# Optimization experiments

Measured on AMD Instinct MI355X. Metric: run time of the kernel, lower is better.

## Reference

```python
import jax, jax.numpy as jnp
import numpy as np
from jax import lax

N_QUBITS = 10
N_LAYERS = 6
DIM = 1 << N_QUBITS
EPS = 1e-5

_i = np.arange(DIM)
# Z_SIGNS[w, i] = (+1/-1) eigenvalue of PauliZ on wire w (wire 0 = most significant bit)
Z_SIGNS = jnp.asarray(np.stack([1.0 - 2.0 * ((_i >> (N_QUBITS - 1 - w)) & 1) for w in range(N_QUBITS)]).astype(np.float32))

def _layer_perm(r):
    # composed permutation of the ring of CNOT(w, (w+r)%n) gates of one StronglyEntanglingLayers layer
    p = _i.copy()
    for w in range(N_QUBITS):
        c, t = w, (w + r) % N_QUBITS
        pc, pt = N_QUBITS - 1 - c, N_QUBITS - 1 - t
        pg = _i ^ (((_i >> pc) & 1) << pt)
        p = p[pg]
    return p

LAYER_PERMS = [jnp.asarray(_layer_perm(l % (N_QUBITS - 1) + 1), dtype=jnp.int32) for l in range(N_LAYERS)]

def _apply_1q(state, U, wire):
    # state: (B, DIM) complex64; U: (2,2) or batched (B,2,2)
    B = state.shape[0]
    left = 1 << wire
    right = DIM // (2 * left)
    s = state.reshape(B, left, 2, right)
    if U.ndim == 3:
        out = jnp.einsum('bij,bljr->blir', U, s)
    else:
        out = jnp.einsum('ij,bljr->blir', U, s)
    return out.reshape(B, DIM)

def _ry_batched(theta):
    c = jnp.cos(theta / 2)
    s = jnp.sin(theta / 2)
    return jnp.stack([jnp.stack([c, -s], -1), jnp.stack([s, c], -1)], -2).astype(jnp.complex64)

def _rot(phi, theta, omega):
    # PennyLane Rot(phi, theta, omega) = RZ(omega) @ RY(theta) @ RZ(phi)
    c = jnp.cos(theta / 2)
    s = jnp.sin(theta / 2)
    m00 = jnp.exp(-1j * (phi + omega) / 2) * c
    m01 = -jnp.exp(1j * (phi - omega) / 2) * s
    m10 = jnp.exp(-1j * (phi - omega) / 2) * s
    m11 = jnp.exp(1j * (phi + omega) / 2) * c
    return jnp.stack([jnp.stack([m00, m01]), jnp.stack([m10, m11])]).astype(jnp.complex64)

def quantum_forward(xq, qw):
    # batched statevector simulation of: RY(pi*x_i) encoding + StronglyEntanglingLayers
    B = xq.shape[0]
    state = jnp.zeros((B, DIM), jnp.complex64).at[:, 0].set(1.0)
    for w in range(N_QUBITS):
        state = _apply_1q(state, _ry_batched(jnp.pi * xq[:, w]), w)
    for l in range(N_LAYERS):
        for w in range(N_QUBITS):
            state = _apply_1q(state, _rot(qw[l, w, 0], qw[l, w, 1], qw[l, w, 2]), w)
        state = state[:, LAYER_PERMS[l]]
    probs = state.real ** 2 + state.imag ** 2
    return probs @ Z_SIGNS.T  # (B, N_QUBITS) expvals of PauliZ

def _conv(x, w, b):
    y = lax.conv_general_dilated(x, w, (1, 1), 'SAME', dimension_numbers=('NCHW', 'OIHW', 'NCHW'))
    return y + b[None, :, None, None]

def _bn(x, g, b):
    # BatchNorm2d in training mode: per-batch statistics over (N, H, W)
    m = jnp.mean(x, (0, 2, 3), keepdims=True)
    v = jnp.var(x, (0, 2, 3), keepdims=True)
    return (x - m) * lax.rsqrt(v + EPS) * g[None, :, None, None] + b[None, :, None, None]

def _pool(x):
    return lax.reduce_window(x, -jnp.inf, lax.max, (1, 1, 2, 2), (1, 1, 2, 2), 'VALID')

def setup_inputs() -> dict:
    key = jax.random.key(0)
    ks = jax.random.split(key, 16)
    n = lambda k, sh, sc: jax.random.normal(k, sh, jnp.float32) * sc
    return {
        'x': jax.random.normal(ks[0], (256, 3, 64, 64), jnp.float32),
        'conv1_w': n(ks[1], (32, 3, 3, 3), 0.1), 'conv1_b': jnp.zeros(32),
        'bn1_g': jnp.ones(32), 'bn1_b': jnp.zeros(32),
        'conv2_w': n(ks[2], (32, 32, 3, 3), 0.05), 'conv2_b': jnp.zeros(32),
        'bn2_g': jnp.ones(32), 'bn2_b': jnp.zeros(32),
        'conv3_w': n(ks[3], (64, 32, 3, 3), 0.05), 'conv3_b': jnp.zeros(64),
        'bn3_g': jnp.ones(64), 'bn3_b': jnp.zeros(64),
        'conv4_w': n(ks[4], (64, 64, 3, 3), 0.05), 'conv4_b': jnp.zeros(64),
        'bn4_g': jnp.ones(64), 'bn4_b': jnp.zeros(64),
        'fc1_w': n(ks[5], (128, 64 * 16 * 16), 0.01), 'fc1_b': jnp.zeros(128),
        'fc2_w': n(ks[6], (10, 128), 0.05), 'fc2_b': jnp.zeros(10),
        'q_weights': jax.random.uniform(ks[7], (6, 10, 3), jnp.float32),
        'head_w': n(ks[8], (10, 10), 0.1), 'head_b': jnp.zeros(10),
    }

def reference(x, conv1_w, conv1_b, bn1_g, bn1_b, conv2_w, conv2_b, bn2_g, bn2_b,
              conv3_w, conv3_b, bn3_g, bn3_b, conv4_w, conv4_b, bn4_g, bn4_b,
              fc1_w, fc1_b, fc2_w, fc2_b, q_weights, head_w, head_b):
    h = jax.nn.relu(_bn(_conv(x, conv1_w, conv1_b), bn1_g, bn1_b))
    h = jax.nn.relu(_bn(_conv(h, conv2_w, conv2_b), bn2_g, bn2_b))
    h = _pool(h)  # Dropout(0.25) is identity in eval
    h = jax.nn.relu(_bn(_conv(h, conv3_w, conv3_b), bn3_g, bn3_b))
    h = jax.nn.relu(_bn(_conv(h, conv4_w, conv4_b), bn4_g, bn4_b))
    h = _pool(h)
    h = h.reshape(h.shape[0], -1)  # (B, 64*16*16)
    h = jax.nn.relu(h @ fc1_w.T + fc1_b)
    h = h @ fc2_w.T + fc2_b  # (B, n_qubits)
    q = quantum_forward(h, q_weights)
    return q @ head_w.T + head_b  # (B, num_classes)
```

## Files before the change

kernel.cpp:

```cpp
#include <hip/hip_runtime.h>
#include <math.h>

#define PI_F 3.14159265358979323846f

typedef __attribute__((ext_vector_type(8))) _Float16 half8;
typedef __attribute__((ext_vector_type(4))) _Float16 half4;
typedef __attribute__((ext_vector_type(4))) float f32x4;

__global__ __launch_bounds__(256) void x_to_nhwc4_kernel(
    const float* __restrict__ x, _Float16* __restrict__ X4)
{
    int idx = blockIdx.x * 256 + threadIdx.x;
    int n = idx >> 11;
    int p = (idx & 2047) * 2;
    const float* xb = x + (size_t)n * 12288;
    float2 c0 = *(const float2*)&xb[p];
    float2 c1 = *(const float2*)&xb[4096 + p];
    float2 c2 = *(const float2*)&xb[8192 + p];
    half8 o;
    o[0] = (_Float16)c0.x; o[1] = (_Float16)c1.x; o[2] = (_Float16)c2.x; o[3] = (_Float16)0.f;
    o[4] = (_Float16)c0.y; o[5] = (_Float16)c1.y; o[6] = (_Float16)c2.y; o[7] = (_Float16)0.f;
    *(half8*)&X4[(size_t)idx * 8] = o;
}

__global__ __launch_bounds__(256) void wt_transform_kernel(
    const float* __restrict__ w1, const float* __restrict__ w2,
    const float* __restrict__ w3, const float* __restrict__ w4,
    _Float16* __restrict__ t1, _Float16* __restrict__ t2,
    _Float16* __restrict__ t3, _Float16* __restrict__ t4)
{
    int idx = blockIdx.x * 256 + threadIdx.x;
    if (idx < 9216) {
        int j = idx & 7, co = (idx >> 3) & 31, k8 = idx >> 8;
        int k = k8 * 8 + j, tap = k >> 5, ci = k & 31;
        t2[idx] = (_Float16)w2[(size_t)(co * 32 + ci) * 9 + tap];
    } else if (idx < 27648) {
        int e = idx - 9216;
        int j = e & 7, co = (e >> 3) & 31, r = e >> 8;
        int k8 = r % 36, gg = r / 36;
        int k = k8 * 8 + j, tap = k >> 5, ci = k & 31;
        t3[e] = (_Float16)w3[(size_t)((gg * 32 + co) * 32 + ci) * 9 + tap];
    } else if (idx < 64512) {
        int e = idx - 27648;
        int j = e & 7, co = (e >> 3) & 31, r = e >> 8;
        int k8 = r % 36, gc = r / 36;
        int g = gc >> 1, cc = gc & 1;
        int kl = k8 * 8 + j, tap = kl >> 5, ci = cc * 32 + (kl & 31);
        t4[e] = (_Float16)w4[(size_t)((g * 32 + co) * 64 + ci) * 9 + tap];
    } else if (idx < 66560) {
        int e = idx - 64512;
        int j = e & 7, co = (e >> 3) & 31, k8 = e >> 8;
        int k = k8 * 8 + j, tap = k >> 2, ci = k & 3;
        t1[e] = (_Float16)((tap < 9 && ci < 3) ? w1[(size_t)(co * 3 + ci) * 9 + tap] : 0.f);
    }
}

__global__ __launch_bounds__(256) void fc1w_transform_kernel(
    const float* __restrict__ w, _Float16* __restrict__ wt)
{
    __shared__ float lds[64][65];
    const int t = threadIdx.x;
    const int yx0 = blockIdx.x * 64;
    const int j = blockIdx.y;
    #pragma unroll
    for (int i = 0; i < 16; ++i) {
        int idx = t + 256 * i;
        int c = idx >> 6, yxl = idx & 63;
        lds[c][yxl] = w[(size_t)j * 16384 + c * 256 + yx0 + yxl];
    }
    __syncthreads();
    #pragma unroll
    for (int i = 0; i < 2; ++i) {
        int idx = t + 256 * i;
        int yxl = idx >> 3, c8 = idx & 7;
        half8 h;
        #pragma unroll
        for (int jj = 0; jj < 8; ++jj)
            h[jj] = (_Float16)lds[c8 * 8 + jj][yxl];
        *(half8*)&wt[(size_t)j * 16384 + (size_t)(yx0 + yxl) * 64 + c8 * 8] = h;
    }
}

__global__ __launch_bounds__(256) void quantum_prep_kernel(
    const float* __restrict__ qw, float* __restrict__ rotm,
    unsigned short* __restrict__ perm)
{
    int t = threadIdx.x;
    if (t < 60) {
        float phi = qw[t * 3], th = qw[t * 3 + 1], om = qw[t * 3 + 2];
        float c = cosf(0.5f * th), s = sinf(0.5f * th);
        float apo = 0.5f * (phi + om), amo = 0.5f * (phi - om);
        float cpo = cosf(apo), spo = sinf(apo);
        float cmo = cosf(amo), smo = sinf(amo);
        rotm[t * 8 + 0] = cpo * c;  rotm[t * 8 + 1] = -spo * c;
        rotm[t * 8 + 2] = -cmo * s; rotm[t * 8 + 3] = -smo * s;
        rotm[t * 8 + 4] = cmo * s;  rotm[t * 8 + 5] = -smo * s;
        rotm[t * 8 + 6] = cpo * c;  rotm[t * 8 + 7] = spo * c;
    }
    for (int e = t; e < 6144; e += 256) {
        int layer = e >> 10, i = e & 1023;
        int r = layer % 9 + 1;
        int jdx = i;
        for (int w = 9; w >= 0; --w) {
            int tt = (w + r) % 10;
            int pc = 9 - w, pt_ = 9 - tt;
            jdx ^= ((jdx >> pc) & 1) << pt_;
        }
        perm[e] = (unsigned short)jdx;
    }
}

__global__ __launch_bounds__(256) void conv1_stats_kernel(
    const _Float16* __restrict__ X4, const _Float16* __restrict__ w1m,
    const float* __restrict__ bias, float* __restrict__ partials)
{
    constexpr int TC = 66, TR = 6;
    constexpr int NPIX = (TR + 1) * TC;
    __shared__ __align__(16) _Float16 s_in[NPIX * 4];
    __shared__ __align__(16) _Float16 s_w[2048];
    __shared__ float s_red[64];

    const int t = threadIdx.x;
    const int row0 = blockIdx.x * 4;
    const int n = blockIdx.z;

    *(half8*)&s_w[t * 8] = *(const half8*)&w1m[t * 8];

    for (int p = t; p < NPIX; p += 256) {
        int col = p % TC, r = p / TC;
        int gy = row0 + r - 1, gx = col - 1;
        uint2 u = make_uint2(0u, 0u);
        if (r < TR && gy >= 0 && gy < 64 && gx >= 0 && gx < 64)
            u = *(const uint2*)&X4[(((size_t)n << 12) + (gy << 6) + gx) * 4];
        *(uint2*)&s_in[p * 4] = u;
    }
    if (t < 64) s_red[t] = 0.f;
    __syncthreads();

    const int w = t >> 6, l = t & 63;
    const int lm = l & 15, lg = l >> 4;
    int pA[4];
    #pragma unroll
    for (int f = 0; f < 4; ++f) {
        int m = w * 64 + f * 16 + lm;
        pA[f] = (m >> 6) * TC + (m & 63);
    }
    f32x4 zero4 = {0.f, 0.f, 0.f, 0.f};
    f32x4 acc[4][2];
    #pragma unroll
    for (int f = 0; f < 4; ++f) { acc[f][0] = zero4; acc[f][1] = zero4; }

    {
        const int t0 = lg * 2;
        const int off0 = (t0 / 3) * TC + (t0 % 3);
        const int off1 = ((t0 + 1) / 3) * TC + ((t0 + 1) % 3);
        half8 b0 = *(const half8*)&s_w[(lg * 32 + lm) * 8];
        half8 b1 = *(const half8*)&s_w[(lg * 32 + 16 + lm) * 8];
        #pragma unroll
        for (int f = 0; f < 4; ++f) {
            half4 alo = *(const half4*)&s_in[(pA[f] + off0) * 4];
            half4 ahi = *(const half4*)&s_in[(pA[f] + off1) * 4];
            half8 a;
            #pragma unroll
            for (int j = 0; j < 4; ++j) { a[j] = alo[j]; a[4 + j] = ahi[j]; }
            acc[f][0] = __builtin_amdgcn_mfma_f32_16x16x32_f16(a, b0, acc[f][0], 0, 0, 0);
            acc[f][1] = __builtin_amdgcn_mfma_f32_16x16x32_f16(a, b1, acc[f][1], 0, 0, 0);
        }
    }
    {
        half8 b0 = *(const half8*)&s_w[((4 + lg) * 32 + lm) * 8];
        half8 b1 = *(const half8*)&s_w[((4 + lg) * 32 + 16 + lm) * 8];
        #pragma unroll
        for (int f = 0; f < 4; ++f) {
            half8 a;
            #pragma unroll
            for (int j = 0; j < 8; ++j) a[j] = (_Float16)0.f;
            if (lg == 0) {
                half4 alo = *(const half4*)&s_in[(pA[f] + 134) * 4];
                half4 ahi = *(const half4*)&s_in[(pA[f] + 198) * 4];
                #pragma unroll
                for (int j = 0; j < 4; ++j) { a[j] = alo[j]; a[4 + j] = ahi[j]; }
            }
            acc[f][0] = __builtin_amdgcn_mfma_f32_16x16x32_f16(a, b0, acc[f][0], 0, 0, 0);
            acc[f][1] = __builtin_amdgcn_mfma_f32_16x16x32_f16(a, b1, acc[f][1], 0, 0, 0);
        }
    }

    float bv0 = bias[lm];
    float bv1 = bias[16 + lm];
    float s0 = 0.f, s20 = 0.f, s1 = 0.f, s21 = 0.f;
    #pragma unroll
    for (int f = 0; f < 4; ++f) {
        #pragma unroll
        for (int r = 0; r < 4; ++r) {
            float v0 = acc[f][0][r] + bv0;
            float v1 = acc[f][1][r] + bv1;
            s0 += v0; s20 += v0 * v0;
            s1 += v1; s21 += v1 * v1;
        }
    }
    s0 += __shfl_xor(s0, 16);  s0 += __shfl_xor(s0, 32);
    s1 += __shfl_xor(s1, 16);  s1 += __shfl_xor(s1, 32);
    s20 += __shfl_xor(s20, 16); s20 += __shfl_xor(s20, 32);
    s21 += __shfl_xor(s21, 16); s21 += __shfl_xor(s21, 32);
    if (l < 16) {
        atomicAdd(&s_red[lm], s0);
        atomicAdd(&s_red[16 + lm], s1);
        atomicAdd(&s_red[32 + lm], s20);
        atomicAdd(&s_red[48 + lm], s21);
    }
    __syncthreads();
    if (t < 64)
        partials[((size_t)n * 16 + blockIdx.x) * 64 + t] = s_red[t];
}

__global__ __launch_bounds__(256, 2) void conv2_fused_kernel(
    const _Float16* __restrict__ X4, const _Float16* __restrict__ w1m,
    const float* __restrict__ c1bias, const _Float16* __restrict__ ssh1,
    const _Float16* __restrict__ wt2, const float* __restrict__ c2bias,
    _Float16* __restrict__ out0, _Float16* __restrict__ out1,
    float* __restrict__ partials)
{
    constexpr int W = 64, COUT = 32, MF = 8, NB = 2;
    constexpr int SPW = MF * 16;
    constexpr int ROWS = 8;
    constexpr int TR = 10, TC = 66, NPIX = TR * TC;
    constexpr int KC = 288;
    constexpr int XC = 68, XROWS = 14, XPIX = XROWS * XC;
    __shared__ __align__(16) _Float16 s_in[NPIX * 32];
    __shared__ __align__(16) _Float16 s_x4[XPIX * 4];
    __shared__ __align__(16) _Float16 s_w1[2048];
    __shared__ float s_red[64];

    const int t = threadIdx.x;
    const int row0 = blockIdx.x * ROWS;
    const int n = blockIdx.z;
    const int w = t >> 6, l = t & 63;
    const int lm = l & 15, lg = l >> 4;

    *(half8*)&s_w1[t * 8] = *(const half8*)&w1m[t * 8];
    for (int p = t; p < XPIX; p += 256) {
        int c = p % XC, r = p / XC;
        int gy = row0 - 2 + r, gx = c - 2;
        uint2 u = make_uint2(0u, 0u);
        if (r < 12 && gy >= 0 && gy < 64 && gx >= 0 && gx < 64)
            u = *(const uint2*)&X4[(((size_t)n << 12) + (gy << 6) + gx) * 4];
        *(uint2*)&s_x4[p * 4] = u;
    }
    if (t < 64) s_red[t] = 0.f;
    __syncthreads();

    {
        const float b1v0 = c1bias[lm], b1v1 = c1bias[16 + lm];
        const _Float16 sc0 = ssh1[lm], sh0 = ssh1[32 + lm];
        const _Float16 sc1 = ssh1[16 + lm], sh1 = ssh1[48 + lm];
        const int c8a = lm >> 3, ja = lm & 7;
        for (int g = w; g < 42; g += 4) {
            int py = g * 16 + lm;
            int ry = py / 66, cy = py - ry * 66;
            int pb = ry * XC + cy;
            f32x4 a0 = {0.f, 0.f, 0.f, 0.f}, a1 = {0.f, 0.f, 0.f, 0.f};
            {
                const int t0 = lg * 2;
                const int off0 = (t0 / 3) * XC + (t0 % 3);
                const int off1 = ((t0 + 1) / 3) * XC + ((t0 + 1) % 3);
                half8 b0 = *(const half8*)&s_w1[(lg * 32 + lm) * 8];
                half8 b1 = *(const half8*)&s_w1[(lg * 32 + 16 + lm) * 8];
                half4 alo = *(const half4*)&s_x4[(pb + off0) * 4];
                half4 ahi = *(const half4*)&s_x4[(pb + off1) * 4];
                half8 a;
                #pragma unroll
                for (int j = 0; j < 4; ++j) { a[j] = alo[j]; a[4 + j] = ahi[j]; }
                a0 = __builtin_amdgcn_mfma_f32_16x16x32_f16(a, b0, a0, 0, 0, 0);
                a1 = __builtin_amdgcn_mfma_f32_16x16x32_f16(a, b1, a1, 0, 0, 0);
            }
            {
                half8 b0 = *(const half8*)&s_w1[((4 + lg) * 32 + lm) * 8];
                half8 b1 = *(const half8*)&s_w1[((4 + lg) * 32 + 16 + lm) * 8];
                half8 a;
                #pragma unroll
                for (int j = 0; j < 8; ++j) a[j] = (_Float16)0.f;
                if (lg == 0) {
                    half4 alo = *(const half4*)&s_x4[(pb + 138) * 4];
                    half4 ahi = *(const half4*)&s_x4[(pb + 204) * 4];
                    #pragma unroll
                    for (int j = 0; j < 4; ++j) { a[j] = alo[j]; a[4 + j] = ahi[j]; }
                }
                a0 = __builtin_amdgcn_mfma_f32_16x16x32_f16(a, b0, a0, 0, 0, 0);
                a1 = __builtin_amdgcn_mfma_f32_16x16x32_f16(a, b1, a1, 0, 0, 0);
            }
            #pragma unroll
            for (int r2 = 0; r2 < 4; ++r2) {
                int py2 = g * 16 + lg * 4 + r2;
                if (py2 < NPIX) {
                    int r2y = py2 / 66, c2y = py2 - r2y * 66;
                    int gy = row0 - 1 + r2y, gx = c2y - 1;
                    _Float16 y0 = (_Float16)0.f, y1 = (_Float16)0.f;
                    if (gy >= 0 && gy < 64 && gx >= 0 && gx < 64) {
                        _Float16 v0 = (_Float16)(a0[r2] + b1v0);
                        _Float16 v1 = (_Float16)(a1[r2] + b1v1);
                        _Float16 f0 = v0 * sc0 + sh0;
                        _Float16 f1 = v1 * sc1 + sh1;
                        y0 = f0 > (_Float16)0.f ? f0 : (_Float16)0.f;
                        y1 = f1 > (_Float16)0.f ? f1 : (_Float16)0.f;
                    }
                    s_in[(c8a * NPIX + py2) * 8 + ja] = y0;
                    s_in[((2 + c8a) * NPIX + py2) * 8 + ja] = y1;
                }
            }
        }
    }
    __syncthreads();

    int pA[MF];
    #pragma unroll
    for (int f = 0; f < MF; ++f) {
        int m = w * SPW + f * 16 + lm;
        pA[f] = (m / W) * TC + (m % W);
    }
    f32x4 zero4 = {0.f, 0.f, 0.f, 0.f};
    f32x4 acc[MF][NB];
    #pragma unroll
    for (int f = 0; f < MF; ++f)
        #pragma unroll
        for (int nb = 0; nb < NB; ++nb) acc[f][nb] = zero4;

    #pragma unroll
    for (int tap = 0; tap < 9; ++tap) {
        const int dy = tap / 3, dx = tap % 3;
        const int poff = dy * TC + dx;
        half8 b[NB];
        #pragma unroll
        for (int nb = 0; nb < NB; ++nb) {
            int col = nb * 16 + lm;
            b[nb] = *(const half8*)&wt2[((tap * 4 + lg) * 32 + col) * 8];
        }
        #pragma unroll
        for (int f = 0; f < MF; ++f) {
            half8 a = *(const half8*)&s_in[(lg * NPIX + pA[f] + poff) * 8];
            #pragma unroll
            for (int nb = 0; nb < NB; ++nb)
                acc[f][nb] = __builtin_amdgcn_mfma_f32_16x16x32_f16(a, b[nb], acc[f][nb], 0, 0, 0);
        }
    }

    float bv[NB], s[NB], s2[NB];
    #pragma unroll
    for (int nb = 0; nb < NB; ++nb) {
        bv[nb] = c2bias[nb * 16 + lm];
        s[nb] = 0.f; s2[nb] = 0.f;
    }
    #pragma unroll
    for (int f = 0; f < MF; ++f) {
        #pragma unroll
        for (int r = 0; r < 4; ++r) {
            #pragma unroll
            for (int nb = 0; nb < NB; ++nb) {
                float v = acc[f][nb][r] + bv[nb];
                s[nb] += v; s2[nb] += v * v;
            }
        }
    }
    #pragma unroll
    for (int nb = 0; nb < NB; ++nb) {
        s[nb] += __shfl_xor(s[nb], 16);  s[nb] += __shfl_xor(s[nb], 32);
        s2[nb] += __shfl_xor(s2[nb], 16); s2[nb] += __shfl_xor(s2[nb], 32);
    }
    if (l < 16) {
        #pragma unroll
        for (int nb = 0; nb < NB; ++nb) {
            atomicAdd(&s_red[nb * 16 + lm], s[nb]);
            atomicAdd(&s_red[32 + nb * 16 + lm], s2[nb]);
        }
    }

    {
        constexpr int FH = MF / 2;
        constexpr int PPIX = (ROWS / 2) * (W / 2);
        __syncthreads();
        _Float16* pk = s_in;
        #pragma unroll
        for (int nb = 0; nb < NB; ++nb) {
            #pragma unroll
            for (int f = 0; f < FH; ++f) {
                #pragma unroll
                for (int rp = 0; rp < 2; ++rp) {
                    float a0 = acc[f][nb][2 * rp] + bv[nb];
                    float a1 = acc[f][nb][2 * rp + 1] + bv[nb];
                    float a2 = acc[f + FH][nb][2 * rp] + bv[nb];
                    float a3 = acc[f + FH][nb][2 * rp + 1] + bv[nb];
                    float mn = fminf(fminf(a0, a1), fminf(a2, a3));
                    float mx = fmaxf(fmaxf(a0, a1), fmaxf(a2, a3));
                    int xp = f * 8 + lg * 2 + rp;
                    int o = (w * (W / 2) + xp) * COUT + nb * 16 + lm;
                    pk[o] = (_Float16)mn;
                    pk[PPIX * COUT + o] = (_Float16)mx;
                }
            }
        }
        __syncthreads();
        size_t gb = (((size_t)n * 32 + (row0 >> 1)) * 32) * COUT;
        for (int idx = t; idx < PPIX * COUT / 8; idx += 256) {
            *(half8*)&out0[gb + (size_t)idx * 8] = *(const half8*)&pk[idx * 8];
            *(half8*)&out1[gb + (size_t)idx * 8] = *(const half8*)&pk[PPIX * COUT + idx * 8];
        }
    }

    __syncthreads();
    if (t < 64) {
        size_t bid = (size_t)n * gridDim.x + blockIdx.x;
        partials[bid * 64 + t] = s_red[t];
    }
}

template<int BLOCK, int W, int CIN, int COUT, int MF, int NB,
         bool MMIN, bool POOL>
__global__ __launch_bounds__(BLOCK, (BLOCK == 512 ? 4 : 3)) void conv_mfma_kernel(
    const _Float16* __restrict__ in0, const _Float16* __restrict__ in1,
    const _Float16* __restrict__ coef, const _Float16* __restrict__ wt,
    const float* __restrict__ bias,
    _Float16* __restrict__ out0, _Float16* __restrict__ out1,
    float* __restrict__ partials)
{
    constexpr int H = W;
    constexpr int NWAVE = BLOCK / 64;
    constexpr int SPW = MF * 16;
    constexpr int ROWS = NWAVE * SPW / W;
    constexpr int TR = ROWS + 2;
    constexpr int TC = W + 2;
    constexpr int NPIX = TR * TC;
    constexpr int NCH = CIN / 32;
    constexpr int C8N = CIN / 8;
    constexpr int KC = 288;
    constexpr int COUTB = NB * 16;
    __shared__ __align__(16) _Float16 s_in[NPIX * CIN];
    __shared__ float s_red[2 * COUTB];

    const int t = threadIdx.x;
    const int row0 = blockIdx.x * ROWS;
    const int n = blockIdx.z;

    const int w = t >> 6, l = t & 63;
    const int lm = l & 15, lg = l >> 4;
    int pA[MF];
    #pragma unroll
    for (int f = 0; f < MF; ++f) {
        int m = w * SPW + f * 16 + lm;
        pA[f] = (m / W) * TC + (m % W);
    }
    f32x4 zero4 = {0.f, 0.f, 0.f, 0.f};
    f32x4 acc[MF][NB];
    #pragma unroll
    for (int f = 0; f < MF; ++f)
        #pragma unroll
        for (int nb = 0; nb < NB; ++nb) acc[f][nb] = zero4;
    if (t < 2 * COUTB) s_red[t] = 0.f;

    for (int idx = t; idx < NPIX * C8N; idx += BLOCK) {
        int c8 = idx % C8N;
        int p = idx / C8N;
        int col = p % TC, r = p / TC;
        int gy = row0 + r - 1, gx = col - 1;
        half8 v;
        #pragma unroll
        for (int j = 0; j < 8; ++j) v[j] = (_Float16)0.f;
        if (gy >= 0 && gy < H && gx >= 0 && gx < W) {
            size_t gidx = (((size_t)n * H + gy) * W + gx) * CIN + c8 * 8;
            if (MMIN) {
                half8 mn = *(const half8*)&in0[gidx];
                half8 mx = *(const half8*)&in1[gidx];
                half8 sa = *(const half8*)&coef[c8 * 8];
                half8 sb = *(const half8*)&coef[CIN + c8 * 8];
                half8 sh = *(const half8*)&coef[2 * CIN + c8 * 8];
                #pragma unroll
                for (int j = 0; j < 8; ++j) {
                    _Float16 f = mx[j] * sa[j] + mn[j] * sb[j] + sh[j];
                    v[j] = f > (_Float16)0.f ? f : (_Float16)0.f;
                }
            } else {
                v = *(const half8*)&in0[gidx];
                if (coef) {
                    half8 sc = *(const half8*)&coef[c8 * 8];
                    half8 sh = *(const half8*)&coef[CIN + c8 * 8];
                    #pragma unroll
                    for (int j = 0; j < 8; ++j) {
                        _Float16 f = v[j] * sc[j] + sh[j];
                        v[j] = f > (_Float16)0.f ? f : (_Float16)0.f;
                    }
                }
            }
        }
        *(half8*)&s_in[(c8 * NPIX + p) * 8] = v;
    }
    __syncthreads();

    #pragma unroll
    for (int tap = 0; tap < 9; ++tap) {
        const int dy = tap / 3, dx = tap % 3;
        const int poff = dy * TC + dx;
        #pragma unroll
        for (int cc = 0; cc < NCH; ++cc) {
            half8 b[NB];
            #pragma unroll
            for (int nb = 0; nb < NB; ++nb) {
                int cog = nb * 16 + lm;
                int gg = cog >> 5, col = cog & 31;
                const _Float16* wp = wt + (size_t)(gg * NCH + cc) * KC * 32;
                b[nb] = *(const half8*)&wp[((tap * 4 + lg) * 32 + col) * 8];
            }
            #pragma unroll
            for (int f = 0; f < MF; ++f) {
                half8 a = *(const half8*)&s_in[((cc * 4 + lg) * NPIX + pA[f] + poff) * 8];
                #pragma unroll
                for (int nb = 0; nb < NB; ++nb)
                    acc[f][nb] = __builtin_amdgcn_mfma_f32_16x16x32_f16(a, b[nb], acc[f][nb], 0, 0, 0);
            }
        }
    }

    float bv[NB], s[NB], s2[NB];
    #pragma unroll
    for (int nb = 0; nb < NB; ++nb) {
        bv[nb] = bias[nb * 16 + lm];
        s[nb] = 0.f; s2[nb] = 0.f;
    }
    #pragma unroll
    for (int f = 0; f < MF; ++f) {
        #pragma unroll
        for (int r = 0; r < 4; ++r) {
            int m = w * SPW + f * 16 + lg * 4 + r;
            int yy = row0 + m / W, xo = m % W;
            size_t base = (((size_t)n * H + yy) * W + xo) * COUT;
            #pragma unroll
            for (int nb = 0; nb < NB; ++nb) {
                float v = acc[f][nb][r] + bv[nb];
                if (!POOL) out0[base + nb * 16 + lm] = (_Float16)v;
                s[nb] += v; s2[nb] += v * v;
            }
        }
    }
    #pragma unroll
    for (int nb = 0; nb < NB; ++nb) {
        s[nb] += __shfl_xor(s[nb], 16);  s[nb] += __shfl_xor(s[nb], 32);
        s2[nb] += __shfl_xor(s2[nb], 16); s2[nb] += __shfl_xor(s2[nb], 32);
    }
    if (l < 16) {
        #pragma unroll
        for (int nb = 0; nb < NB; ++nb) {
            atomicAdd(&s_red[nb * 16 + lm], s[nb]);
            atomicAdd(&s_red[COUTB + nb * 16 + lm], s2[nb]);
        }
    }

    if (POOL) {
        constexpr int FH = MF / 2;
        constexpr int PPIX = (ROWS / 2) * (W / 2);
        static_assert(2 * PPIX * COUT <= NPIX * CIN, "pool pack fits in s_in");
        __syncthreads();
        _Float16* pk = s_in;
        #pragma unroll
        for (int nb = 0; nb < NB; ++nb) {
            #pragma unroll
            for (int f = 0; f < FH; ++f) {
                #pragma unroll
                for (int rp = 0; rp < 2; ++rp) {
                    float a0 = acc[f][nb][2 * rp] + bv[nb];
                    float a1 = acc[f][nb][2 * rp + 1] + bv[nb];
                    float a2 = acc[f + FH][nb][2 * rp] + bv[nb];
                    float a3 = acc[f + FH][nb][2 * rp + 1] + bv[nb];
                    float mn = fminf(fminf(a0, a1), fminf(a2, a3));
                    float mx = fmaxf(fmaxf(a0, a1), fmaxf(a2, a3));
                    int xp = f * 8 + lg * 2 + rp;
                    int o = (w * (W / 2) + xp) * COUT + nb * 16 + lm;
                    pk[o] = (_Float16)mn;
                    pk[PPIX * COUT + o] = (_Float16)mx;
                }
            }
        }
        __syncthreads();
        size_t gb = (((size_t)n * (H / 2) + (row0 >> 1)) * (W / 2)) * COUT;
        for (int idx = t; idx < PPIX * COUT / 8; idx += BLOCK) {
            *(half8*)&out0[gb + (size_t)idx * 8] = *(const half8*)&pk[idx * 8];
            *(half8*)&out1[gb + (size_t)idx * 8] = *(const half8*)&pk[(PPIX * COUT + idx * 8)];
        }
    }

    __syncthreads();
    if (t < 2 * COUTB) {
        size_t bid = (size_t)n * gridDim.x + blockIdx.x;
        partials[bid * 2 * COUTB + t] = s_red[t];
    }
}

__global__ __launch_bounds__(256) void bn_finalize_kernel(
    const float* __restrict__ partials, int nx, float inv_count,
    const float* __restrict__ gamma, const float* __restrict__ beta,
    float* __restrict__ ss, _Float16* __restrict__ ssh,
    _Float16* __restrict__ sab, int COUT)
{
    const int c = blockIdx.x;
    const int t = threadIdx.x;
    float sum = 0.f, sq = 0.f;
    int total = 256 * nx;
    for (int e = t; e < total; e += 256) {
        size_t off = (size_t)e * 2 * COUT;
        sum += partials[off + c];
        sq  += partials[off + COUT + c];
    }
    #pragma unroll
    for (int off = 32; off > 0; off >>= 1) {
        sum += __shfl_xor(sum, off);
        sq  += __shfl_xor(sq, off);
    }
    __shared__ float rs[4], rq[4];
    if ((t & 63) == 0) { rs[t >> 6] = sum; rq[t >> 6] = sq; }
    __syncthreads();
    if (t == 0) {
        sum = rs[0] + rs[1] + rs[2] + rs[3];
        sq  = rq[0] + rq[1] + rq[2] + rq[3];
        float mean = sum * inv_count;
        float var = sq * inv_count - mean * mean;
        float scale = gamma[c] * rsqrtf(var + 1e-5f);
        float shift = beta[c] - mean * scale;
        ss[c] = scale;
        ss[COUT + c] = shift;
        if (ssh) {
            ssh[c] = (_Float16)scale;
            ssh[COUT + c] = (_Float16)shift;
        }
        if (sab) {
            sab[c] = (_Float16)(scale > 0.f ? scale : 0.f);
            sab[COUT + c] = (_Float16)(scale > 0.f ? 0.f : scale);
            sab[2 * COUT + c] = (_Float16)shift;
        }
    }
}

__global__ __launch_bounds__(256) void fc1_mfma_kernel(
    const _Float16* __restrict__ Amin, const _Float16* __restrict__ Amax,
    const _Float16* __restrict__ sab, const _Float16* __restrict__ Bw,
    float* __restrict__ hp)
{
    __shared__ __align__(16) _Float16 As[64][72];
    __shared__ __align__(16) _Float16 Bs[128][72];
    const int t = threadIdx.x;
    const int mt = blockIdx.x;
    const int kc = blockIdx.y;
    const int w = t >> 6, l = t & 63;
    const int lm = l & 15, lg = l >> 4;

    f32x4 zero4 = {0.f, 0.f, 0.f, 0.f};
    f32x4 acc[8];
    #pragma unroll
    for (int nb = 0; nb < 8; ++nb) acc[nb] = zero4;

    const size_t a_base = (size_t)(mt * 64) * 16384 + (size_t)kc * 512;
    const size_t b_base = (size_t)kc * 512;

    for (int p = 0; p < 8; ++p) {
        __syncthreads();
        #pragma unroll
        for (int i = 0; i < 2; ++i) {
            int idx = t + 256 * i;
            int r = idx >> 3, c8 = idx & 7;
            size_t off = a_base + (size_t)r * 16384 + p * 64 + c8 * 8;
            half8 mn = *(const half8*)&Amin[off];
            half8 mx = *(const half8*)&Amax[off];
            half8 sa = *(const half8*)&sab[c8 * 8];
            half8 sb = *(const half8*)&sab[64 + c8 * 8];
            half8 sh = *(const half8*)&sab[128 + c8 * 8];
            half8 v;
            #pragma unroll
            for (int j = 0; j < 8; ++j) {
                _Float16 f = mx[j] * sa[j] + mn[j] * sb[j] + sh[j];
                v[j] = f > (_Float16)0.f ? f : (_Float16)0.f;
            }
            *(half8*)&As[r][c8 * 8] = v;
        }
        #pragma unroll
        for (int i = 0; i < 4; ++i) {
            int idx = t + 256 * i;
            int r = idx >> 3, c8 = idx & 7;
            *(half8*)&Bs[r][c8 * 8] =
                *(const half8*)&Bw[b_base + (size_t)r * 16384 + p * 64 + c8 * 8];
        }
        __syncthreads();
        #pragma unroll
        for (int ks = 0; ks < 64; ks += 32) {
            half8 a = *(const half8*)&As[w * 16 + lm][ks + lg * 8];
            #pragma unroll
            for (int nb = 0; nb < 8; ++nb) {
                half8 b = *(const half8*)&Bs[nb * 16 + lm][ks + lg * 8];
                acc[nb] = __builtin_amdgcn_mfma_f32_16x16x32_f16(a, b, acc[nb], 0, 0, 0);
            }
        }
    }
    #pragma unroll
    for (int nb = 0; nb < 8; ++nb) {
        #pragma unroll
        for (int r = 0; r < 4; ++r) {
            int row = mt * 64 + w * 16 + lg * 4 + r;
            hp[((size_t)kc * 256 + row) * 128 + nb * 16 + lm] = acc[nb][r];
        }
    }
}

__global__ __launch_bounds__(256) void fc1_reduce_kernel(
    const float* __restrict__ hp, const float* __restrict__ bias, float* __restrict__ h1)
{
    int gid = blockIdx.x * 256 + threadIdx.x;
    int n = gid >> 7, j = gid & 127;
    float s = bias[j];
    #pragma unroll
    for (int kc = 0; kc < 32; ++kc) s += hp[((size_t)kc * 256 + n) * 128 + j];
    h1[gid] = fmaxf(0.f, s);
}

__global__ __launch_bounds__(64) void fc2_kernel(
    const float* __restrict__ h1, const float* __restrict__ w,
    const float* __restrict__ b, float* __restrict__ xq)
{
    int n = blockIdx.x, l = threadIdx.x;
    float a0 = h1[n * 128 + l], a1 = h1[n * 128 + 64 + l];
    float p[10];
    #pragma unroll
    for (int j = 0; j < 10; ++j)
        p[j] = w[j * 128 + l] * a0 + w[j * 128 + 64 + l] * a1;
    #pragma unroll
    for (int j = 0; j < 10; ++j) {
        #pragma unroll
        for (int off = 32; off > 0; off >>= 1) p[j] += __shfl_xor(p[j], off);
    }
    if (l == 0) {
        #pragma unroll
        for (int j = 0; j < 10; ++j) xq[n * 10 + j] = p[j] + b[j];
    }
}

__global__ __launch_bounds__(64) void quantum_head_kernel(
    const float* __restrict__ xq, const float* __restrict__ rotm,
    const unsigned short* __restrict__ perm,
    const float* __restrict__ head_w, const float* __restrict__ head_b,
    float* __restrict__ outp)
{
    __shared__ float lds[2048];
    const int n = blockIdx.x;
    const int l = threadIdx.x;

    float ar[16], ai[16];
    #pragma unroll
    for (int r = 0; r < 16; ++r) { ar[r] = 0.f; ai[r] = 0.f; }
    if (l == 0) ar[0] = 1.f;

    #pragma unroll
    for (int w = 0; w < 10; ++w) {
        float th = 0.5f * PI_F * xq[n * 10 + w];
        float c = cosf(th), s = sinf(th);
        const int k = 9 - w;
        if (k >= 6) {
            const int b = k - 6;
            #pragma unroll
            for (int r = 0; r < 16; ++r) {
                if (!(r & (1 << b))) {
                    int r1 = r | (1 << b);
                    float a0 = ar[r], a1 = ar[r1];
                    ar[r]  = c * a0 - s * a1;
                    ar[r1] = s * a0 + c * a1;
                }
            }
        } else {
            float ss = ((l >> k) & 1) ? s : -s;
            #pragma unroll
            for (int r = 0; r < 16; ++r) {
                float p = __shfl_xor(ar[r], 1 << k);
                ar[r] = c * ar[r] + ss * p;
            }
        }
    }

    #pragma unroll 1
    for (int layer = 0; layer < 6; ++layer) {
        #pragma unroll
        for (int w = 0; w < 10; ++w) {
            const float* m = rotm + (layer * 10 + w) * 8;
            float m00r = m[0], m00i = m[1], m01r = m[2], m01i = m[3];
            float m10r = m[4], m10i = m[5], m11r = m[6], m11i = m[7];
            const int k = 9 - w;
            if (k >= 6) {
                const int b = k - 6;
                #pragma unroll
                for (int r = 0; r < 16; ++r) {
                    if (!(r & (1 << b))) {
                        int r1 = r | (1 << b);
                        float a0r = ar[r], a0i = ai[r];
                        float a1r = ar[r1], a1i = ai[r1];
                        ar[r]  = m00r * a0r - m00i * a0i + m01r * a1r - m01i * a1i;
                        ai[r]  = m00r * a0i + m00i * a0r + m01r * a1i + m01i * a1r;
                        ar[r1] = m10r * a0r - m10i * a0i + m11r * a1r - m11i * a1i;
                        ai[r1] = m10r * a0i + m10i * a0r + m11r * a1i + m11i * a1r;
                    }
                }
            } else {
                int bit = (l >> k) & 1;
                float mAr = bit ? m11r : m00r, mAi = bit ? m11i : m00i;
                float mBr = bit ? m10r : m01r, mBi = bit ? m10i : m01i;
                #pragma unroll
                for (int r = 0; r < 16; ++r) {
                    float pr = __shfl_xor(ar[r], 1 << k);
                    float pi = __shfl_xor(ai[r], 1 << k);
                    float mr = ar[r], mi = ai[r];
                    ar[r] = mAr * mr - mAi * mi + mBr * pr - mBi * pi;
                    ai[r] = mAr * mi + mAi * mr + mBr * pi + mBi * pr;
                }
            }
        }
        #pragma unroll
        for (int r = 0; r < 16; ++r) {
            lds[(r << 6) | l] = ar[r];
            lds[1024 + ((r << 6) | l)] = ai[r];
        }
        __syncthreads();
        const unsigned short* pt = perm + layer * 1024;
        #pragma unroll
        for (int r = 0; r < 16; ++r) {
            int ji = pt[(r << 6) | l];
            ar[r] = lds[ji];
            ai[r] = lds[1024 + ji];
        }
        __syncthreads();
    }

    float S = 0.f, T0 = 0.f, T1 = 0.f, T2 = 0.f, T3 = 0.f;
    #pragma unroll
    for (int r = 0; r < 16; ++r) {
        float pr = ar[r] * ar[r] + ai[r] * ai[r];
        S += pr;
        T0 += (r & 1) ? -pr : pr;
        T1 += (r & 2) ? -pr : pr;
        T2 += (r & 4) ? -pr : pr;
        T3 += (r & 8) ? -pr : pr;
    }
    float pk[10];
    pk[0] = T3; pk[1] = T2; pk[2] = T1; pk[3] = T0;
    #pragma unroll
    for (int w = 4; w < 10; ++w)
        pk[w] = ((l >> (9 - w)) & 1) ? -S : S;
    #pragma unroll
    for (int w = 0; w < 10; ++w) {
        #pragma unroll
        for (int off = 1; off < 64; off <<= 1)
            pk[w] += __shfl_xor(pk[w], off);
    }
    if (l < 10) {
        float o = head_b[l];
        #pragma unroll
        for (int kk = 0; kk < 10; ++kk) o += pk[kk] * head_w[l * 10 + kk];
        outp[n * 10 + l] = o;
    }
}

extern "C" void kernel_launch(void* const* d_in, const int* in_sizes, int n_in,
                              void* d_out, int out_size, void* d_ws, size_t ws_size,
                              hipStream_t stream)
{
    const float* x   = (const float*)d_in[0];
    const float* c1w = (const float*)d_in[1];  const float* c1b = (const float*)d_in[2];
    const float* g1  = (const float*)d_in[3];  const float* b1  = (const float*)d_in[4];
    const float* c2w = (const float*)d_in[5];  const float* c2b = (const float*)d_in[6];
    const float* g2  = (const float*)d_in[7];  const float* b2  = (const float*)d_in[8];
    const float* c3w = (const float*)d_in[9];  const float* c3b = (const float*)d_in[10];
    const float* g3  = (const float*)d_in[11]; const float* b3  = (const float*)d_in[12];
    const float* c4w = (const float*)d_in[13]; const float* c4b = (const float*)d_in[14];
    const float* g4  = (const float*)d_in[15]; const float* b4  = (const float*)d_in[16];
    const float* f1w = (const float*)d_in[17]; const float* f1b = (const float*)d_in[18];
    const float* f2w = (const float*)d_in[19]; const float* f2b = (const float*)d_in[20];
    const float* qw  = (const float*)d_in[21];
    const float* hw  = (const float*)d_in[22]; const float* hb  = (const float*)d_in[23];

    float* ws = (float*)d_ws;
    _Float16* H0 = (_Float16*)ws;
    _Float16* H1 = H0 + 33554432;
    float* part = ws + 33554432;
    float* ss1  = part + 524288;
    float* ss2  = ss1 + 64;
    float* ss3  = ss2 + 64;
    float* ss4  = ss3 + 128;
    float* hp   = ss4 + 128;
    float* h1   = hp + 1048576;
    float* xqv  = h1 + 32768;
    float* rotm = xqv + 2560;
    unsigned short* perm16 = (unsigned short*)(rotm + 480);
    _Float16* ssh1 = (_Float16*)(perm16 + 6144);
    _Float16* ssh3 = ssh1 + 64;
    _Float16* sab2 = ssh3 + 128;
    _Float16* sab4 = sab2 + 96;
    _Float16* wt2  = sab4 + 192;
    _Float16* wt3  = wt2 + 9216;
    _Float16* wt4  = wt3 + 18432;
    _Float16* w1m  = wt4 + 36864;
    _Float16* w1t  = w1m + 2048;
    _Float16* X4   = w1t + 2097152;

    _Float16* minT2 = H1;
    _Float16* maxT2 = H1 + 8388608;
    _Float16* minT4 = H1;
    _Float16* maxT4 = H1 + 4194304;

    quantum_prep_kernel<<<1, 256, 0, stream>>>(qw, rotm, perm16);
    wt_transform_kernel<<<260, 256, 0, stream>>>(c1w, c2w, c3w, c4w, w1m, wt2, wt3, wt4);
    fc1w_transform_kernel<<<dim3(4, 128), 256, 0, stream>>>(f1w, w1t);
    x_to_nhwc4_kernel<<<2048, 256, 0, stream>>>(x, X4);

    conv1_stats_kernel<<<dim3(16, 1, 256), 256, 0, stream>>>(X4, w1m, c1b, part);
    bn_finalize_kernel<<<32, 256, 0, stream>>>(part, 16, 1.f / 1048576.f,
                                               g1, b1, ss1, ssh1, nullptr, 32);

    conv2_fused_kernel<<<dim3(8, 1, 256), 256, 0, stream>>>(
        X4, w1m, c1b, ssh1, wt2, c2b, minT2, maxT2, part);
    bn_finalize_kernel<<<32, 256, 0, stream>>>(part, 8, 1.f / 1048576.f,
                                               g2, b2, ss2, nullptr, sab2, 32);

    conv_mfma_kernel<512, 32, 32, 64, 4, 4, true, false>
        <<<dim3(2, 1, 256), 512, 0, stream>>>(
        minT2, maxT2, sab2, wt3, c3b, H0, nullptr, part);
    bn_finalize_kernel<<<64, 256, 0, stream>>>(part, 2, 1.f / 262144.f,
                                               g3, b3, ss3, ssh3, nullptr, 64);

    conv_mfma_kernel<512, 32, 64, 64, 4, 4, false, true>
        <<<dim3(2, 1, 256), 512, 0, stream>>>(
        H0, nullptr, ssh3, wt4, c4b, minT4, maxT4, part);
    bn_finalize_kernel<<<64, 256, 0, stream>>>(part, 2, 1.f / 262144.f,
                                               g4, b4, ss4, nullptr, sab4, 64);

    fc1_mfma_kernel<<<dim3(4, 32), 256, 0, stream>>>(minT4, maxT4, sab4, w1t, hp);
    fc1_reduce_kernel<<<128, 256, 0, stream>>>(hp, f1b, h1);

    fc2_kernel<<<256, 64, 0, stream>>>(h1, f2w, f2b, xqv);

    quantum_head_kernel<<<256, 64, 0, stream>>>(xqv, rotm, perm16, hw, hb, (float*)d_out);
}
```

Baseline: 214.6 us.

## Merge prep kernels, fuse fc1-reduce with fc2, and halve conv2 row tiles

Four preprocessing kernels become one launch that branches on block index, and the fc1 reduction and fc2 are fused into one kernel with LDS staging, removing three launches and the h1 round trip. The fused conv2 kernel now handles 4 rows per block instead of 8, with a smaller LDS footprint and launch bounds raised to 4 blocks per CU, doubling the grid. The 2x2 pooling is split into a horizontal min/max in registers and a vertical min/max during the store. Smaller tiles add halo recompute of conv1 and increase partial-statistic rows in exchange for higher occupancy.

```diff
diff --git a/kernel.cpp b/kernel.cpp
--- a/kernel.cpp
+++ b/kernel.cpp
@@ -7,106 +7,100 @@
 typedef __attribute__((ext_vector_type(4))) _Float16 half4;
 typedef __attribute__((ext_vector_type(4))) float f32x4;
 
-__global__ __launch_bounds__(256) void x_to_nhwc4_kernel(
-    const float* __restrict__ x, _Float16* __restrict__ X4)
-{
-    int idx = blockIdx.x * 256 + threadIdx.x;
-    int n = idx >> 11;
-    int p = (idx & 2047) * 2;
-    const float* xb = x + (size_t)n * 12288;
-    float2 c0 = *(const float2*)&xb[p];
-    float2 c1 = *(const float2*)&xb[4096 + p];
-    float2 c2 = *(const float2*)&xb[8192 + p];
-    half8 o;
-    o[0] = (_Float16)c0.x; o[1] = (_Float16)c1.x; o[2] = (_Float16)c2.x; o[3] = (_Float16)0.f;
-    o[4] = (_Float16)c0.y; o[5] = (_Float16)c1.y; o[6] = (_Float16)c2.y; o[7] = (_Float16)0.f;
-    *(half8*)&X4[(size_t)idx * 8] = o;
-}
-
-__global__ __launch_bounds__(256) void wt_transform_kernel(
+__global__ __launch_bounds__(256) void prep_kernel(
+    const float* __restrict__ x, _Float16* __restrict__ X4,
     const float* __restrict__ w1, const float* __restrict__ w2,
     const float* __restrict__ w3, const float* __restrict__ w4,
     _Float16* __restrict__ t1, _Float16* __restrict__ t2,
-    _Float16* __restrict__ t3, _Float16* __restrict__ t4)
-{
-    int idx = blockIdx.x * 256 + threadIdx.x;
-    if (idx < 9216) {
-        int j = idx & 7, co = (idx >> 3) & 31, k8 = idx >> 8;
-        int k = k8 * 8 + j, tap = k >> 5, ci = k & 31;
-        t2[idx] = (_Float16)w2[(size_t)(co * 32 + ci) * 9 + tap];
-    } else if (idx < 27648) {
-        int e = idx - 9216;
-        int j = e & 7, co = (e >> 3) & 31, r = e >> 8;
-        int k8 = r % 36, gg = r / 36;
-        int k = k8 * 8 + j, tap = k >> 5, ci = k & 31;
-        t3[e] = (_Float16)w3[(size_t)((gg * 32 + co) * 32 + ci) * 9 + tap];
-    } else if (idx < 64512) {
-        int e = idx - 27648;
-        int j = e & 7, co = (e >> 3) & 31, r = e >> 8;
-        int k8 = r % 36, gc = r / 36;
-        int g = gc >> 1, cc = gc & 1;
-        int kl = k8 * 8 + j, tap = kl >> 5, ci = cc * 32 + (kl & 31);
-        t4[e] = (_Float16)w4[(size_t)((g * 32 + co) * 64 + ci) * 9 + tap];
-    } else if (idx < 66560) {
-        int e = idx - 64512;
-        int j = e & 7, co = (e >> 3) & 31, k8 = e >> 8;
-        int k = k8 * 8 + j, tap = k >> 2, ci = k & 3;
-        t1[e] = (_Float16)((tap < 9 && ci < 3) ? w1[(size_t)(co * 3 + ci) * 9 + tap] : 0.f);
-    }
-}
-
-__global__ __launch_bounds__(256) void fc1w_transform_kernel(
-    const float* __restrict__ w, _Float16* __restrict__ wt)
-{
-    __shared__ float lds[64][65];
-    const int t = threadIdx.x;
-    const int yx0 = blockIdx.x * 64;
-    const int j = blockIdx.y;
-    #pragma unroll
-    for (int i = 0; i < 16; ++i) {
-        int idx = t + 256 * i;
-        int c = idx >> 6, yxl = idx & 63;
-        lds[c][yxl] = w[(size_t)j * 16384 + c * 256 + yx0 + yxl];
-    }
-    __syncthreads();
-    #pragma unroll
-    for (int i = 0; i < 2; ++i) {
-        int idx = t + 256 * i;
-        int yxl = idx >> 3, c8 = idx & 7;
-        half8 h;
-        #pragma unroll
-        for (int jj = 0; jj < 8; ++jj)
-            h[jj] = (_Float16)lds[c8 * 8 + jj][yxl];
-        *(half8*)&wt[(size_t)j * 16384 + (size_t)(yx0 + yxl) * 64 + c8 * 8] = h;
-    }
-}
-
-__global__ __launch_bounds__(256) void quantum_prep_kernel(
+    _Float16* __restrict__ t3, _Float16* __restrict__ t4,
+    const float* __restrict__ f1w, _Float16* __restrict__ w1t,
     const float* __restrict__ qw, float* __restrict__ rotm,
     unsigned short* __restrict__ perm)
 {
-    int t = threadIdx.x;
-    if (t < 60) {
-        float phi = qw[t * 3], th = qw[t * 3 + 1], om = qw[t * 3 + 2];
-        float c = cosf(0.5f * th), s = sinf(0.5f * th);
-        float apo = 0.5f * (phi + om), amo = 0.5f * (phi - om);
-        float cpo = cosf(apo), spo = sinf(apo);
-        float cmo = cosf(amo), smo = sinf(amo);
-        rotm[t * 8 + 0] = cpo * c;  rotm[t * 8 + 1] = -spo * c;
-        rotm[t * 8 + 2] = -cmo * s; rotm[t * 8 + 3] = -smo * s;
-        rotm[t * 8 + 4] = cmo * s;  rotm[t * 8 + 5] = -smo * s;
-        rotm[t * 8 + 6] = cpo * c;  rotm[t * 8 + 7] = spo * c;
-    }
-    for (int e = t; e < 6144; e += 256) {
-        int layer = e >> 10, i = e & 1023;
-        int r = layer % 9 + 1;
-        int jdx = i;
-        for (int w = 9; w >= 0; --w) {
-            int tt = (w + r) % 10;
-            int pc = 9 - w, pt_ = 9 - tt;
-            jdx ^= ((jdx >> pc) & 1) << pt_;
-        }
-        perm[e] = (unsigned short)jdx;
+    const int b = blockIdx.x;
+    const int t = threadIdx.x;
+    if (b < 2048) {
+        int idx = b * 256 + t;
+        int n = idx >> 11;
+        int p = (idx & 2047) * 2;
+        const float* xb = x + (size_t)n * 12288;
+        float2 c0 = *(const float2*)&xb[p];
+        float2 c1 = *(const float2*)&xb[4096 + p];
+        float2 c2 = *(const float2*)&xb[8192 + p];
+        half8 o;
+        o[0] = (_Float16)c0.x; o[1] = (_Float16)c1.x; o[2] = (_Float16)c2.x; o[3] = (_Float16)0.f;
+        o[4] = (_Float16)c0.y; o[5] = (_Float16)c1.y; o[6] = (_Float16)c2.y; o[7] = (_Float16)0.f;
+        *(half8*)&X4[(size_t)idx * 8] = o;
+    } else if (b < 2308) {
+        int idx = (b - 2048) * 256 + t;
+        if (idx < 9216) {
+            int j = idx & 7, co = (idx >> 3) & 31, k8 = idx >> 8;
+            int k = k8 * 8 + j, tap = k >> 5, ci = k & 31;
+            t2[idx] = (_Float16)w2[(size_t)(co * 32 + ci) * 9 + tap];
+        } else if (idx < 27648) {
+            int e = idx - 9216;
+            int j = e & 7, co = (e >> 3) & 31, r = e >> 8;
+            int k8 = r % 36, gg = r / 36;
+            int k = k8 * 8 + j, tap = k >> 5, ci = k & 31;
+            t3[e] = (_Float16)w3[(size_t)((gg * 32 + co) * 32 + ci) * 9 + tap];
+        } else if (idx < 64512) {
+            int e = idx - 27648;
+            int j = e & 7, co = (e >> 3) & 31, r = e >> 8;
+            int k8 = r % 36, gc = r / 36;
+            int g = gc >> 1, cc = gc & 1;
+            int kl = k8 * 8 + j, tap = kl >> 5, ci = cc * 32 + (kl & 31);
+            t4[e] = (_Float16)w4[(size_t)((g * 32 + co) * 64 + ci) * 9 + tap];
+        } else if (idx < 66560) {
+            int e = idx - 64512;
+            int j = e & 7, co = (e >> 3) & 31, k8 = e >> 8;
+            int k = k8 * 8 + j, tap = k >> 2, ci = k & 3;
+            t1[e] = (_Float16)((tap < 9 && ci < 3) ? w1[(size_t)(co * 3 + ci) * 9 + tap] : 0.f);
+        }
+    } else if (b < 2820) {
+        __shared__ float lds[64][65];
+        int b2 = b - 2308;
+        const int yx0 = (b2 & 3) * 64;
+        const int j = b2 >> 2;
+        #pragma unroll
+        for (int i = 0; i < 16; ++i) {
+            int idx = t + 256 * i;
+            int c = idx >> 6, yxl = idx & 63;
+            lds[c][yxl] = f1w[(size_t)j * 16384 + c * 256 + yx0 + yxl];
+        }
+        __syncthreads();
+        #pragma unroll
+        for (int i = 0; i < 2; ++i) {
+            int idx = t + 256 * i;
+            int yxl = idx >> 3, c8 = idx & 7;
+            half8 h;
+            #pragma unroll
+            for (int jj = 0; jj < 8; ++jj)
+                h[jj] = (_Float16)lds[c8 * 8 + jj][yxl];
+            *(half8*)&w1t[(size_t)j * 16384 + (size_t)(yx0 + yxl) * 64 + c8 * 8] = h;
+        }
+    } else {
+        if (t < 60) {
+            float phi = qw[t * 3], th = qw[t * 3 + 1], om = qw[t * 3 + 2];
+            float c = cosf(0.5f * th), s = sinf(0.5f * th);
+            float apo = 0.5f * (phi + om), amo = 0.5f * (phi - om);
+            float cpo = cosf(apo), spo = sinf(apo);
+            float cmo = cosf(amo), smo = sinf(amo);
+            rotm[t * 8 + 0] = cpo * c;  rotm[t * 8 + 1] = -spo * c;
+            rotm[t * 8 + 2] = -cmo * s; rotm[t * 8 + 3] = -smo * s;
+            rotm[t * 8 + 4] = cmo * s;  rotm[t * 8 + 5] = -smo * s;
+            rotm[t * 8 + 6] = cpo * c;  rotm[t * 8 + 7] = spo * c;
+        }
+        for (int e = t; e < 6144; e += 256) {
+            int layer = e >> 10, i = e & 1023;
+            int r = layer % 9 + 1;
+            int jdx = i;
+            for (int w = 9; w >= 0; --w) {
+                int tt = (w + r) % 10;
+                int pc = 9 - w, pt_ = 9 - tt;
+                jdx ^= ((jdx >> pc) & 1) << pt_;
+            }
+            perm[e] = (unsigned short)jdx;
+        }
     }
 }
 
@@ -214,19 +208,17 @@
         partials[((size_t)n * 16 + blockIdx.x) * 64 + t] = s_red[t];
 }
 
-__global__ __launch_bounds__(256, 2) void conv2_fused_kernel(
+__global__ __launch_bounds__(256, 4) void conv2_fused_kernel(
     const _Float16* __restrict__ X4, const _Float16* __restrict__ w1m,
     const float* __restrict__ c1bias, const _Float16* __restrict__ ssh1,
     const _Float16* __restrict__ wt2, const float* __restrict__ c2bias,
     _Float16* __restrict__ out0, _Float16* __restrict__ out1,
     float* __restrict__ partials)
 {
-    constexpr int W = 64, COUT = 32, MF = 8, NB = 2;
-    constexpr int SPW = MF * 16;
-    constexpr int ROWS = 8;
-    constexpr int TR = 10, TC = 66, NPIX = TR * TC;
-    constexpr int KC = 288;
-    constexpr int XC = 68, XROWS = 14, XPIX = XROWS * XC;
+    constexpr int W = 64, COUT = 32, MF = 4, NB = 2;
+    constexpr int ROWS = 4;
+    constexpr int TC = 66, NPIX = 6 * 66;
+    constexpr int XC = 68, XPIX = 9 * 68;
     __shared__ __align__(16) _Float16 s_in[NPIX * 32];
     __shared__ __align__(16) _Float16 s_x4[XPIX * 4];
     __shared__ __align__(16) _Float16 s_w1[2048];
@@ -243,7 +235,7 @@
         int c = p % XC, r = p / XC;
         int gy = row0 - 2 + r, gx = c - 2;
         uint2 u = make_uint2(0u, 0u);
-        if (r < 12 && gy >= 0 && gy < 64 && gx >= 0 && gx < 64)
+        if (gy >= 0 && gy < 64 && gx >= 0 && gx < 64)
             u = *(const uint2*)&X4[(((size_t)n << 12) + (gy << 6) + gx) * 4];
         *(uint2*)&s_x4[p * 4] = u;
     }
@@ -255,9 +247,10 @@
         const _Float16 sc0 = ssh1[lm], sh0 = ssh1[32 + lm];
         const _Float16 sc1 = ssh1[16 + lm], sh1 = ssh1[48 + lm];
         const int c8a = lm >> 3, ja = lm & 7;
-        for (int g = w; g < 42; g += 4) {
+        for (int g = w; g < 25; g += 4) {
             int py = g * 16 + lm;
-            int ry = py / 66, cy = py - ry * 66;
+            int pyc = py < NPIX ? py : 0;
+            int ry = pyc / 66, cy = pyc - ry * 66;
             int pb = ry * XC + cy;
             f32x4 a0 = {0.f, 0.f, 0.f, 0.f}, a1 = {0.f, 0.f, 0.f, 0.f};
             {
@@ -314,10 +307,8 @@
 
     int pA[MF];
     #pragma unroll
-    for (int f = 0; f < MF; ++f) {
-        int m = w * SPW + f * 16 + lm;
-        pA[f] = (m / W) * TC + (m % W);
-    }
+    for (int f = 0; f < MF; ++f)
+        pA[f] = w * TC + f * 16 + lm;
     f32x4 zero4 = {0.f, 0.f, 0.f, 0.f};
     f32x4 acc[MF][NB];
     #pragma unroll
@@ -375,35 +366,39 @@
     }
 
     {
-        constexpr int FH = MF / 2;
-        constexpr int PPIX = (ROWS / 2) * (W / 2);
         __syncthreads();
         _Float16* pk = s_in;
         #pragma unroll
         for (int nb = 0; nb < NB; ++nb) {
             #pragma unroll
-            for (int f = 0; f < FH; ++f) {
+            for (int f = 0; f < MF; ++f) {
                 #pragma unroll
                 for (int rp = 0; rp < 2; ++rp) {
                     float a0 = acc[f][nb][2 * rp] + bv[nb];
                     float a1 = acc[f][nb][2 * rp + 1] + bv[nb];
-                    float a2 = acc[f + FH][nb][2 * rp] + bv[nb];
-                    float a3 = acc[f + FH][nb][2 * rp + 1] + bv[nb];
-                    float mn = fminf(fminf(a0, a1), fminf(a2, a3));
-                    float mx = fmaxf(fmaxf(a0, a1), fmaxf(a2, a3));
                     int xp = f * 8 + lg * 2 + rp;
-                    int o = (w * (W / 2) + xp) * COUT + nb * 16 + lm;
-                    pk[o] = (_Float16)mn;
-                    pk[PPIX * COUT + o] = (_Float16)mx;
+                    int o = (w * 32 + xp) * COUT + nb * 16 + lm;
+                    pk[o] = (_Float16)fminf(a0, a1);
+                    pk[4096 + o] = (_Float16)fmaxf(a0, a1);
                 }
             }
         }
         __syncthreads();
-        size_t gb = (((size_t)n * 32 + (row0 >> 1)) * 32) * COUT;
-        for (int idx = t; idx < PPIX * COUT / 8; idx += 256) {
-            *(half8*)&out0[gb + (size_t)idx * 8] = *(const half8*)&pk[idx * 8];
-            *(half8*)&out1[gb + (size_t)idx * 8] = *(const half8*)&pk[PPIX * COUT + idx * 8];
-        }
+        int hp_row = t >> 7, rem = t & 127;
+        int xp = rem >> 2, c8 = rem & 3;
+        half8 mnA = *(const half8*)&pk[((2 * hp_row) * 32 + xp) * COUT + c8 * 8];
+        half8 mnB = *(const half8*)&pk[((2 * hp_row + 1) * 32 + xp) * COUT + c8 * 8];
+        half8 mxA = *(const half8*)&pk[4096 + ((2 * hp_row) * 32 + xp) * COUT + c8 * 8];
+        half8 mxB = *(const half8*)&pk[4096 + ((2 * hp_row + 1) * 32 + xp) * COUT + c8 * 8];
+        half8 mn, mx;
+        #pragma unroll
+        for (int j = 0; j < 8; ++j) {
+            mn[j] = mnA[j] < mnB[j] ? mnA[j] : mnB[j];
+            mx[j] = mxA[j] > mxB[j] ? mxA[j] : mxB[j];
+        }
+        size_t ob = (((size_t)n * 32 + (row0 >> 1) + hp_row) * 32 + xp) * COUT + c8 * 8;
+        *(half8*)&out0[ob] = mn;
+        *(half8*)&out1[ob] = mx;
     }
 
     __syncthreads();
@@ -705,35 +700,24 @@
     }
 }
 
-__global__ __launch_bounds__(256) void fc1_reduce_kernel(
-    const float* __restrict__ hp, const float* __restrict__ bias, float* __restrict__ h1)
+__global__ __launch_bounds__(128) void fc12_kernel(
+    const float* __restrict__ hp, const float* __restrict__ f1b,
+    const float* __restrict__ f2w, const float* __restrict__ f2b,
+    float* __restrict__ xq)
 {
-    int gid = blockIdx.x * 256 + threadIdx.x;
-    int n = gid >> 7, j = gid & 127;
-    float s = bias[j];
+    __shared__ float hl[128];
+    const int n = blockIdx.x;
+    const int j = threadIdx.x;
+    float s = f1b[j];
     #pragma unroll
     for (int kc = 0; kc < 32; ++kc) s += hp[((size_t)kc * 256 + n) * 128 + j];
-    h1[gid] = fmaxf(0.f, s);
-}
-
-__global__ __launch_bounds__(64) void fc2_kernel(
-    const float* __restrict__ h1, const float* __restrict__ w,
-    const float* __restrict__ b, float* __restrict__ xq)
-{
-    int n = blockIdx.x, l = threadIdx.x;
-    float a0 = h1[n * 128 + l], a1 = h1[n * 128 + 64 + l];
-    float p[10];
-    #pragma unroll
-    for (int j = 0; j < 10; ++j)
-        p[j] = w[j * 128 + l] * a0 + w[j * 128 + 64 + l] * a1;
-    #pragma unroll
-    for (int j = 0; j < 10; ++j) {
-        #pragma unroll
-        for (int off = 32; off > 0; off >>= 1) p[j] += __shfl_xor(p[j], off);
-    }
-    if (l == 0) {
-        #pragma unroll
-        for (int j = 0; j < 10; ++j) xq[n * 10 + j] = p[j] + b[j];
+    hl[j] = fmaxf(0.f, s);
+    __syncthreads();
+    if (j < 10) {
+        float o = f2b[j];
+        #pragma unroll 4
+        for (int k = 0; k < 128; ++k) o += f2w[j * 128 + k] * hl[k];
+        xq[n * 10 + j] = o;
     }
 }
 
@@ -886,8 +870,7 @@
     float* ss3  = ss2 + 64;
     float* ss4  = ss3 + 128;
     float* hp   = ss4 + 128;
-    float* h1   = hp + 1048576;
-    float* xqv  = h1 + 32768;
+    float* xqv  = hp + 1048576;
     float* rotm = xqv + 2560;
     unsigned short* perm16 = (unsigned short*)(rotm + 480);
     _Float16* ssh1 = (_Float16*)(perm16 + 6144);
@@ -906,18 +889,17 @@
     _Float16* minT4 = H1;
     _Float16* maxT4 = H1 + 4194304;
 
-    quantum_prep_kernel<<<1, 256, 0, stream>>>(qw, rotm, perm16);
-    wt_transform_kernel<<<260, 256, 0, stream>>>(c1w, c2w, c3w, c4w, w1m, wt2, wt3, wt4);
-    fc1w_transform_kernel<<<dim3(4, 128), 256, 0, stream>>>(f1w, w1t);
-    x_to_nhwc4_kernel<<<2048, 256, 0, stream>>>(x, X4);
+    prep_kernel<<<2821, 256, 0, stream>>>(x, X4, c1w, c2w, c3w, c4w,
+                                          w1m, wt2, wt3, wt4, f1w, w1t,
+                                          qw, rotm, perm16);
 
     conv1_stats_kernel<<<dim3(16, 1, 256), 256, 0, stream>>>(X4, w1m, c1b, part);
     bn_finalize_kernel<<<32, 256, 0, stream>>>(part, 16, 1.f / 1048576.f,
                                                g1, b1, ss1, ssh1, nullptr, 32);
 
-    conv2_fused_kernel<<<dim3(8, 1, 256), 256, 0, stream>>>(
+    conv2_fused_kernel<<<dim3(16, 1, 256), 256, 0, stream>>>(
         X4, w1m, c1b, ssh1, wt2, c2b, minT2, maxT2, part);
-    bn_finalize_kernel<<<32, 256, 0, stream>>>(part, 8, 1.f / 1048576.f,
+    bn_finalize_kernel<<<32, 256, 0, stream>>>(part, 16, 1.f / 1048576.f,
                                                g2, b2, ss2, nullptr, sab2, 32);
 
     conv_mfma_kernel<512, 32, 32, 64, 4, 4, true, false>
@@ -933,9 +915,7 @@
                                                g4, b4, ss4, nullptr, sab4, 64);
 
     fc1_mfma_kernel<<<dim3(4, 32), 256, 0, stream>>>(minT4, maxT4, sab4, w1t, hp);
-    fc1_reduce_kernel<<<128, 256, 0, stream>>>(hp, f1b, h1);
-
-    fc2_kernel<<<256, 64, 0, stream>>>(h1, f2w, f2b, xqv);
+    fc12_kernel<<<256, 128, 0, stream>>>(hp, f1b, f2w, f2b, xqv);
 
     quantum_head_kernel<<<256, 64, 0, stream>>>(xqv, rotm, perm16, hw, hb, (float*)d_out);
 }
```

Measured after the change: 205.7 us. 4.1% less time.
